# Kernel tuning notes

Hardware: AMD Instinct MI355X
Metric: run time of the kernel (lower is better)

The kernel has to match this reference:

```python
import jax, jax.numpy as jnp
import numpy as np

B, H, W, C = 4, 448, 448, 3
P = 16
G = 28            # grid = H // P
T = G * G         # 784 patches
E = 768
HD = 3072
NH = 12
DH = E // NH
L = 6
LW = 9            # local_window


def _ln(x, g, b, eps=1e-5):
    m = x.mean(-1, keepdims=True)
    v = ((x - m) ** 2).mean(-1, keepdims=True)
    return (x - m) / jnp.sqrt(v + eps) * g + b


def _mask_bias():
    # torch bool attn_mask: True = disallowed. The module sets True for LOCAL
    # neighbors (|dr|<=lw//2 and |dc|<=lw//2), so local positions are MASKED OUT.
    idx = jnp.arange(T)
    r, c = idx // G, idx % G
    local = (jnp.abs(r[:, None] - r[None, :]) <= LW // 2) & \
            (jnp.abs(c[:, None] - c[None, :]) <= LW // 2)
    return jnp.where(local, -jnp.inf, 0.0).astype(jnp.float32)  # [T, T]


def _img_to_patch(x):
    # x: [B,H,W,C] -> [B,T,C*P*P], channel-major within a patch (matches torch code)
    x = x.transpose(0, 3, 1, 2)                       # [B,C,H,W]
    x = x.reshape(B, C, G, P, G, P)
    x = x.transpose(0, 2, 4, 1, 3, 5)                 # [B,G,G,C,P,P]
    return x.reshape(B, T, C * P * P)


def _forward(x, sxr_mean, sxr_std, input_w, input_b, pos_emb,
             ln1_w, ln1_b, in_w, in_b, out_w, out_b, ln2_w, ln2_b,
             w1, b1, w2, b2, head_ln_w, head_ln_b, head_w, head_b):
    h = _img_to_patch(x) @ input_w.T + input_b        # [B,T,E]
    h = (h.reshape(B, G, G, E) + pos_emb).reshape(B, T, E)
    bias = _mask_bias()

    def block(h, prm):
        l1w, l1b, iw, ib, ow, ob, l2w, l2b, W1, B1, W2, B2 = prm
        y = _ln(h, l1w, l1b)
        qkv = y @ iw.T + ib                           # [B,T,3E]
        q, k, v = jnp.split(qkv, 3, axis=-1)
        q = q.reshape(B, T, NH, DH)
        k = k.reshape(B, T, NH, DH)
        v = v.reshape(B, T, NH, DH)
        s = jnp.einsum('bqhd,bkhd->bhqk', q, k) / jnp.sqrt(jnp.float32(DH)) + bias
        a = jax.nn.softmax(s, axis=-1)
        o = jnp.einsum('bhqk,bkhd->bqhd', a, v).reshape(B, T, E)
        h = h + o @ ow.T + ob
        y2 = _ln(h, l2w, l2b)
        m = jax.nn.gelu(y2 @ W1.T + B1, approximate=False)  # torch nn.GELU default
        h = h + m @ W2.T + B2
        return h, None

    h, _ = jax.lax.scan(block, h, (ln1_w, ln1_b, in_w, in_b, out_w, out_b,
                                   ln2_w, ln2_b, w1, b1, w2, b2))

    logits = (_ln(h, head_ln_w, head_ln_b) @ head_w.T + head_b)[..., 0]  # [B,T]
    patch_flux = jnp.clip(10.0 ** (logits * sxr_std[0] + sxr_mean[0]) - 1e-8,
                          1e-15, 1.0)
    global_flux = jnp.maximum(patch_flux.sum(axis=1, keepdims=True), 1e-15)
    return global_flux, patch_flux


def setup_inputs() -> dict:
    key = jax.random.key(0)
    ks = iter(jax.random.split(key, 16))
    def p(shape, s=0.02):
        return jax.random.normal(next(ks), shape, jnp.float32) * s
    return dict(
        x=jax.random.normal(next(ks), (B, H, W, C), jnp.float32),
        sxr_mean=jnp.array([-6.0], jnp.float32),
        sxr_std=jnp.array([1.0], jnp.float32),
        input_w=p((E, C * P * P)), input_b=jnp.zeros(E, jnp.float32),
        pos_emb=p((1, G, G, E), 1.0),
        ln1_w=jnp.ones((L, E), jnp.float32), ln1_b=jnp.zeros((L, E), jnp.float32),
        in_w=p((L, 3 * E, E)), in_b=jnp.zeros((L, 3 * E), jnp.float32),
        out_w=p((L, E, E)), out_b=jnp.zeros((L, E), jnp.float32),
        ln2_w=jnp.ones((L, E), jnp.float32), ln2_b=jnp.zeros((L, E), jnp.float32),
        w1=p((L, HD, E)), b1=jnp.zeros((L, HD), jnp.float32),
        w2=p((L, E, HD)), b2=jnp.zeros((L, E), jnp.float32),
        head_ln_w=jnp.ones(E, jnp.float32), head_ln_b=jnp.zeros(E, jnp.float32),
        head_w=p((1, E)), head_b=jnp.zeros(1, jnp.float32),
    )


def reference(x, sxr_mean, sxr_std, input_w, input_b, pos_emb,
              ln1_w, ln1_b, in_w, in_b, out_w, out_b, ln2_w, ln2_b,
              w1, b1, w2, b2, head_ln_w, head_ln_b, head_w, head_b):
    return _forward(x, sxr_mean, sxr_std, input_w, input_b, pos_emb,
                    ln1_w, ln1_b, in_w, in_b, out_w, out_b, ln2_w, ln2_b,
                    w1, b1, w2, b2, head_ln_w, head_ln_b, head_w, head_b)
```

## Files before the change

### kernel.cpp

```cpp
#include <hip/hip_runtime.h>
#include <math.h>

#define BB 4
#define TT 784
#define GG 28
#define EE 768
#define HDIM 3072
#define NHEAD 12
#define NLAYER 6
#define TTP 832
#define PSL (3136 * 768)

typedef short bfrag __attribute__((ext_vector_type(8)));
typedef float ffrag __attribute__((ext_vector_type(4)));

__device__ __forceinline__ unsigned short f2b(float f) {
    union { float f; unsigned u; } v; v.f = f;
    unsigned r = v.u + 0x7FFF + ((v.u >> 16) & 1);
    return (unsigned short)(r >> 16);
}

__device__ __forceinline__ float fexp2(float x) {
    float r; asm("v_exp_f32 %0, %1" : "=v"(r) : "v"(x)); return r;
}
__device__ __forceinline__ float frcp(float x) {
    float r; asm("v_rcp_f32 %0, %1" : "=v"(r) : "v"(x)); return r;
}

#define GLOAD_LDS16(g, l)                                                          \
    __builtin_amdgcn_global_load_lds(                                              \
        (const __attribute__((address_space(1))) void*)(g),                        \
        (__attribute__((address_space(3))) void*)(l), 16, 0, 0)

__device__ __forceinline__ void swz_bxyz(int& bx, int& by, int& bz) {
    int gx = gridDim.x, gy = gridDim.y, gz = gridDim.z;
    int nwg = gx * gy * gz;
    int orig = blockIdx.x + gx * (blockIdx.y + gy * blockIdx.z);
    int q = nwg >> 3, r = nwg & 7;
    int xc = orig & 7, li = orig >> 3;
    int wg = (xc < r ? xc * (q + 1) : r * (q + 1) + (xc - r) * q) + li;
    bx = wg % gx;
    int t = wg / gx;
    by = t % gy;
    bz = t / gy;
}

__device__ __forceinline__ float block_reduce_sum256(float v, volatile float* sb) {
    #pragma unroll
    for (int m = 1; m < 64; m <<= 1) v += __shfl_xor(v, m, 64);
    int wave = threadIdx.x >> 6;
    if ((threadIdx.x & 63) == 0) sb[wave] = v;
    __syncthreads();
    return sb[0] + sb[1] + sb[2] + sb[3];
}

__device__ __forceinline__ float block_reduce_sum192(float v, volatile float* sb) {
    #pragma unroll
    for (int m = 1; m < 64; m <<= 1) v += __shfl_xor(v, m, 64);
    int wave = threadIdx.x >> 6;
    if ((threadIdx.x & 63) == 0) sb[wave] = v;
    __syncthreads();
    return sb[0] + sb[1] + sb[2];
}

__global__ __launch_bounds__(256) void cast_kernel(const float* __restrict__ s,
                                                   unsigned short* __restrict__ d, int n4) {
    int i = blockIdx.x * 256 + threadIdx.x;
    if (i >= n4) return;
    float4 v = ((const float4*)s)[i];
    ushort4 o;
    o.x = f2b(v.x); o.y = f2b(v.y); o.z = f2b(v.z); o.w = f2b(v.w);
    ((ushort4*)d)[i] = o;
}

__global__ __launch_bounds__(256) void fused_cast_kernel(const float* __restrict__ iw,
                                                         const float* __restrict__ ow,
                                                         const float* __restrict__ W1,
                                                         const float* __restrict__ W2,
                                                         unsigned short* __restrict__ dq,
                                                         unsigned short* __restrict__ doo,
                                                         unsigned short* __restrict__ d1,
                                                         unsigned short* __restrict__ d2) {
    int i = blockIdx.x * 256 + threadIdx.x;
    const float* s; unsigned short* d; int k;
    if (i < 442368)            { s = iw;  d = dq;  k = i; }
    else if (i < 589824)       { s = ow;  d = doo; k = i - 442368; }
    else if (i < 1179648)      { s = W1;  d = d1;  k = i - 589824; }
    else if (i < 1769472)      { s = W2;  d = d2;  k = i - 1179648; }
    else return;
    float4 v = ((const float4*)s)[k];
    ushort4 o;
    o.x = f2b(v.x); o.y = f2b(v.y); o.z = f2b(v.z); o.w = f2b(v.w);
    ((ushort4*)d)[k] = o;
}

__global__ __launch_bounds__(256) void patchify_kernel(const float* __restrict__ x,
                                                       unsigned short* __restrict__ P) {
    int idx = blockIdx.x * blockDim.x + threadIdx.x;
    const int total = BB * TT * EE;
    if (idx >= total) return;
    int k = idx % EE;
    int t = (idx / EE) % TT;
    int b = idx / (EE * TT);
    int c = k >> 8;
    int rem = k & 255;
    int p1 = rem >> 4;
    int p2 = rem & 15;
    int g1 = t / GG, g2 = t % GG;
    int hh = g1 * 16 + p1, ww = g2 * 16 + p2;
    P[idx] = f2b(x[((b * 448 + hh) * 448 + ww) * 3 + c]);
}

__global__ __launch_bounds__(256) void posfill_kernel(float* __restrict__ h,
                                                      const float* __restrict__ pos) {
    int idx = blockIdx.x * blockDim.x + threadIdx.x;
    const int total = BB * TT * EE;
    if (idx >= total) return;
    h[idx] = pos[idx % (TT * EE)];
}

__global__ __launch_bounds__(256) void mask_build_kernel(unsigned long long* __restrict__ mt) {
    int idx = blockIdx.x * 256 + threadIdx.x;
    if (idx >= TT * 13) return;
    int row = idx / 13, t = idx % 13;
    int qr = row / GG, qc = row % GG;
    unsigned long long bits = 0;
    for (int i = 0; i < 64; i++) {
        int k = t * 64 + i;
        bool m;
        if (k >= TT) m = true;
        else {
            int kr2 = k / GG, kc2 = k % GG;
            m = (abs(qr - kr2) <= 4) && (abs(qc - kc2) <= 4);
        }
        if (m) bits |= (1ull << i);
    }
    mt[idx] = bits;
}

__global__ __launch_bounds__(192) void ln_red_kernel(float* __restrict__ H,
                                                     const float* __restrict__ P,
                                                     const float* __restrict__ g,
                                                     const float* __restrict__ bt,
                                                     unsigned short* __restrict__ Yb,
                                                     float* __restrict__ Yf) {
    __shared__ float sb1[3];
    __shared__ float sb2[3];
    int row = blockIdx.x, tid = threadIdx.x;
    size_t base = (size_t)row * EE + tid * 4;
    float4 hv = *(float4*)(H + base);
    float4 p0 = *(const float4*)(P + base);
    float4 p1 = *(const float4*)(P + (size_t)PSL + base);
    float4 p2 = *(const float4*)(P + 2 * (size_t)PSL + base);
    float4 p3 = *(const float4*)(P + 3 * (size_t)PSL + base);
    hv.x += (p0.x + p1.x) + (p2.x + p3.x);
    hv.y += (p0.y + p1.y) + (p2.y + p3.y);
    hv.z += (p0.z + p1.z) + (p2.z + p3.z);
    hv.w += (p0.w + p1.w) + (p2.w + p3.w);
    *(float4*)(H + base) = hv;
    float s = block_reduce_sum192((hv.x + hv.y) + (hv.z + hv.w), sb1);
    float mean = s * (1.0f / 768.0f);
    float dx = hv.x - mean, dy = hv.y - mean, dz = hv.z - mean, dw = hv.w - mean;
    __syncthreads();
    float ss = block_reduce_sum192((dx * dx + dy * dy) + (dz * dz + dw * dw), sb2);
    float rstd = rsqrtf(ss * (1.0f / 768.0f) + 1e-5f);
    float4 gv = *(const float4*)(g + tid * 4);
    float4 bv = *(const float4*)(bt + tid * 4);
    float y0 = dx * rstd * gv.x + bv.x;
    float y1 = dy * rstd * gv.y + bv.y;
    float y2 = dz * rstd * gv.z + bv.z;
    float y3 = dw * rstd * gv.w + bv.w;
    ushort4 o;
    o.x = f2b(y0); o.y = f2b(y1); o.z = f2b(y2); o.w = f2b(y3);
    *(ushort4*)(Yb + base) = o;
    if (Yf) {
        float4 yf; yf.x = y0; yf.y = y1; yf.z = y2; yf.w = y3;
        *(float4*)(Yf + base) = yf;
    }
}

__device__ __forceinline__ void gemm_core(const unsigned short* __restrict__ A,
                                          const unsigned short* __restrict__ W,
                                          int M, int K, int m0, int n0,
                                          int kbeg, int nk,
                                          unsigned short* As,
                                          unsigned short* Ws,
                                          ffrag (&acc)[4][4]) {
    int tid = threadIdx.x;
    int wave = tid >> 6, lane = tid & 63;
    int cl = lane & 15, qd = lane >> 4;
    int sr  = lane >> 2;
    int sbk = lane & 3;
    int ssc = (sbk ^ (sr & 3)) << 3;
    int mh = (wave & 1) << 6, nh = (wave >> 1) << 6;

    const unsigned short* Asrc0;
    const unsigned short* Asrc1;
    const unsigned short* Wsrc0;
    const unsigned short* Wsrc1;
    {
        int ar0 = m0 + (wave << 5) + sr;       if (ar0 > M - 1) ar0 = M - 1;
        int ar1 = m0 + (wave << 5) + 16 + sr;  if (ar1 > M - 1) ar1 = M - 1;
        Asrc0 = A + (size_t)ar0 * K + kbeg + ssc;
        Asrc1 = A + (size_t)ar1 * K + kbeg + ssc;
        int wr0 = n0 + (wave << 5) + sr;
        int wr1 = n0 + (wave << 5) + 16 + sr;
        Wsrc0 = W + (size_t)wr0 * K + kbeg + ssc;
        Wsrc1 = W + (size_t)wr1 * K + kbeg + ssc;
    }
    int dof0 = (wave << 10);
    int dof1 = (wave << 10) + 512;
    int fo = (qd ^ (cl & 3)) << 3;

#define STAGE32(sa, sw, kk) do {                         \
        GLOAD_LDS16(Asrc0 + (kk), (sa) + dof0);          \
        GLOAD_LDS16(Asrc1 + (kk), (sa) + dof1);          \
        GLOAD_LDS16(Wsrc0 + (kk), (sw) + dof0);          \
        GLOAD_LDS16(Wsrc1 + (kk), (sw) + dof1);          \
    } while (0)

    unsigned short *a0 = As, *a1 = As + 4096, *a2 = As + 8192;
    unsigned short *w0 = Ws, *w1 = Ws + 4096, *w2 = Ws + 8192;

    STAGE32(a0, w0, 0);
    if (nk > 1) STAGE32(a1, w1, 32);

    for (int t = 0; t < nk; ++t) {
        if (t + 2 < nk) {
            STAGE32(a2, w2, (t + 2) << 5);
            asm volatile("s_waitcnt vmcnt(8)" ::: "memory");
        } else if (t + 1 < nk) {
            asm volatile("s_waitcnt vmcnt(4)" ::: "memory");
        } else {
            asm volatile("s_waitcnt vmcnt(0)" ::: "memory");
        }
        __builtin_amdgcn_s_barrier();
        __builtin_amdgcn_sched_barrier(0);

        bfrag af[4], bf[4];
        #pragma unroll
        for (int i = 0; i < 4; i++)
            af[i] = *(const bfrag*)&a0[((mh + (i << 4) + cl) << 5) + fo];
        #pragma unroll
        for (int j = 0; j < 4; j++)
            bf[j] = *(const bfrag*)&w0[((nh + (j << 4) + cl) << 5) + fo];
        __builtin_amdgcn_s_setprio(1);
        #pragma unroll
        for (int i = 0; i < 4; i++)
            #pragma unroll
            for (int j = 0; j < 4; j++)
                acc[i][j] = __builtin_amdgcn_mfma_f32_16x16x32_bf16(af[i], bf[j], acc[i][j], 0, 0, 0);
        __builtin_amdgcn_s_setprio(0);

        __builtin_amdgcn_s_barrier();
        unsigned short* tp;
        tp = a0; a0 = a1; a1 = a2; a2 = tp;
        tp = w0; w0 = w1; w1 = w2; w2 = tp;
    }
#undef STAGE32
}

__global__ __launch_bounds__(256) void gemm_bf16(const unsigned short* __restrict__ A,
                                                 const unsigned short* __restrict__ W,
                                                 const float* __restrict__ bias,
                                                 const float* R, float* C,
                                                 unsigned short* Cb,
                                                 int M, int N, int K, int act) {
    __shared__ __align__(16) unsigned short As[3 * 4096];
    __shared__ __align__(16) unsigned short Ws[3 * 4096];
    int bx, by, bz;
    swz_bxyz(bx, by, bz);
    int m0 = by << 7, n0 = bx << 7;

    ffrag acc[4][4] = {};
    gemm_core(A, W, M, K, m0, n0, 0, K >> 5, As, Ws, acc);

    int tid = threadIdx.x;
    int wave = tid >> 6, lane = tid & 63;
    int cl = lane & 15, qd = lane >> 4;
    int mh = (wave & 1) << 6, nh = (wave >> 1) << 6;

    #pragma unroll
    for (int j = 0; j < 4; j++) {
        int col = n0 + nh + (j << 4) + cl;
        float bv = bias[col];
        #pragma unroll
        for (int i = 0; i < 4; i++) {
            int row0 = m0 + mh + (i << 4) + (qd << 2);
            #pragma unroll
            for (int r = 0; r < 4; r++) {
                int row = row0 + r;
                if (row < M) {
                    float v = acc[i][j][r] + bv;
                    if (R) v += R[(size_t)row * N + col];
                    if (act) v = 0.5f * v * (1.0f + erff(v * 0.70710678118654752f));
                    if (C)  C[(size_t)row * N + col] = v;
                    if (Cb) Cb[(size_t)row * N + col] = f2b(v);
                }
            }
        }
    }
}

__global__ __launch_bounds__(256) void gemm_qkv(const unsigned short* __restrict__ A,
                                                const unsigned short* __restrict__ W,
                                                const float* __restrict__ bias,
                                                unsigned short* __restrict__ Q,
                                                unsigned short* __restrict__ Kd,
                                                unsigned short* __restrict__ vT,
                                                int M, int N, int K) {
    __shared__ __align__(16) unsigned short As[3 * 4096];
    __shared__ __align__(16) unsigned short Ws[3 * 4096];
    int bx, by, bz;
    swz_bxyz(bx, by, bz);
    int m0 = by << 7, n0 = bx << 7;

    ffrag acc[4][4] = {};
    gemm_core(A, W, M, K, m0, n0, 0, K >> 5, As, Ws, acc);

    int tid = threadIdx.x;
    int wave = tid >> 6, lane = tid & 63;
    int cl = lane & 15, qd = lane >> 4;
    int mh = (wave & 1) << 6, nh = (wave >> 1) << 6;

    int ncb = n0 + nh;
    if (ncb < 1536) {
        unsigned short* dst = (ncb < 768) ? Q : Kd;
        int cb = (ncb < 768) ? 0 : 768;
        #pragma unroll
        for (int j = 0; j < 4; j++) {
            int col = ncb + (j << 4) + cl;
            float bv = bias[col];
            #pragma unroll
            for (int i = 0; i < 4; i++) {
                int row0 = m0 + mh + (i << 4) + (qd << 2);
                #pragma unroll
                for (int r = 0; r < 4; r++) {
                    int row = row0 + r;
                    if (row < M)
                        dst[(size_t)row * EE + col - cb] = f2b(acc[i][j][r] + bv);
                }
            }
        }
    } else {
        int hh = (ncb - 1536) >> 6;
        #pragma unroll
        for (int i = 0; i < 4; i++) {
            int row0 = m0 + mh + (i << 4) + (qd << 2);
            #pragma unroll
            for (int r = 0; r < 4; r++) {
                int row = row0 + r;
                if (row < M) {
                    int b = row / TT;
                    int t = row - b * TT;
                    size_t vbase = ((size_t)(b * NHEAD + hh) * 64) * TTP + t;
                    #pragma unroll
                    for (int j = 0; j < 4; j++) {
                        int col = ncb + (j << 4) + cl;
                        vT[vbase + (size_t)((j << 4) + cl) * TTP] =
                            f2b(acc[i][j][r] + bias[col]);
                    }
                }
            }
        }
    }
}

__global__ __launch_bounds__(256) void gemm_bf16_pk(const unsigned short* __restrict__ A,
                                                    const unsigned short* __restrict__ W,
                                                    const float* __restrict__ bias,
                                                    float* __restrict__ Pp,
                                                    int M, int N, int K, int KC) {
    __shared__ __align__(16) unsigned short As[3 * 4096];
    __shared__ __align__(16) unsigned short Ws[3 * 4096];
    int bx, by, bz;
    swz_bxyz(bx, by, bz);
    int m0 = by << 7, n0 = bx << 7;
    int z = bz;
    int kbeg = z * KC;
    int kc2 = (kbeg + KC > K) ? (K - kbeg) : KC;

    ffrag acc[4][4] = {};
    gemm_core(A, W, M, K, m0, n0, kbeg, kc2 >> 5, As, Ws, acc);

    int tid = threadIdx.x;
    int wave = tid >> 6, lane = tid & 63;
    int cl = lane & 15, qd = lane >> 4;
    int mh = (wave & 1) << 6, nh = (wave >> 1) << 6;
    float* Cz = Pp + (size_t)z * M * N;

    #pragma unroll
    for (int j = 0; j < 4; j++) {
        int col = n0 + nh + (j << 4) + cl;
        float bv = (z == 0) ? bias[col] : 0.0f;
        #pragma unroll
        for (int i = 0; i < 4; i++) {
            int row0 = m0 + mh + (i << 4) + (qd << 2);
            #pragma unroll
            for (int r = 0; r < 4; r++) {
                int row = row0 + r;
                if (row < M)
                    Cz[(size_t)row * N + col] = acc[i][j][r] + bv;
            }
        }
    }
}

#define LP 72
#define SCL2 0.18033688011112042f
__global__ __launch_bounds__(256) void attn_kernel(const unsigned short* __restrict__ Qg,
                                                   const unsigned short* __restrict__ Kg,
                                                   const unsigned short* __restrict__ vT,
                                                   const unsigned long long* __restrict__ mtab,
                                                   unsigned short* __restrict__ O) {
    __shared__ unsigned short Ks[64 * LP];
    __shared__ unsigned short Vt[80 * LP];
    __shared__ unsigned short Pb[64 * LP];
    int tid = threadIdx.x;
    int wave = tid >> 6, lane = tid & 63;
    int cl = lane & 15, qd = lane >> 4;
    int bx, by, bz;
    swz_bxyz(bx, by, bz);
    int bh = by;
    int b = bh / NHEAD, hh = bh % NHEAD;
    int q0 = bx * 64;
    int qw = q0 + wave * 16;

    for (int i = tid; i < 16 * LP; i += 256)
        Vt[64 * LP + i] = (i < LP) ? (unsigned short)0x3F80 : (unsigned short)0;

    int qrow = qw + cl;
    if (qrow > TT - 1) qrow = TT - 1;
    const unsigned short* qb = Qg + (size_t)(b * TT + qrow) * EE + hh * 64;
    bfrag qf0 = *(const bfrag*)(qb + (qd << 3));
    bfrag qf1 = *(const bfrag*)(qb + 32 + (qd << 3));

    ffrag o_acc[5] = {};
    float m_run[4];
    int qg_[4], qm_[4];
    #pragma unroll
    for (int r = 0; r < 4; r++) {
        qg_[r] = qw + (qd << 2) + r;
        qm_[r] = qg_[r] > TT - 1 ? TT - 1 : qg_[r];
        m_run[r] = -1e30f;
    }

    const unsigned short* kbase = Kg + (size_t)b * TT * EE + hh * 64;
    const unsigned short* vbase = vT + (size_t)(b * NHEAD + hh) * 64 * TTP;
    int srow = tid >> 3;
    int scol = (tid & 7) << 3;
    int r0 = srow, r1 = 32 + srow;
    const unsigned short* vp0 = vbase + (size_t)r0 * TTP + scol;
    const unsigned short* vp1 = vbase + (size_t)r1 * TTP + scol;

    bfrag kreg0 = *(const bfrag*)(kbase + (size_t)r0 * EE + scol);
    bfrag kreg1 = *(const bfrag*)(kbase + (size_t)r1 * EE + scol);
    bfrag vreg0 = *(const bfrag*)vp0;
    bfrag vreg1 = *(const bfrag*)vp1;

    int rot = (cl >> 2) & 3;
    int pread0 = (wave * 16 + cl) * LP + ((((qd >> 1)    ) ^ rot) << 4) + ((qd & 1) << 3);
    int pread1 = (wave * 16 + cl) * LP + (((2 + (qd >> 1)) ^ rot) << 4) + ((qd & 1) << 3);

    for (int k0 = 0; k0 < 832; k0 += 64) {
        __syncthreads();
        *(bfrag*)&Ks[r0 * LP + scol] = kreg0;
        *(bfrag*)&Ks[r1 * LP + scol] = kreg1;
        *(bfrag*)&Vt[r0 * LP + scol] = vreg0;
        *(bfrag*)&Vt[r1 * LP + scol] = vreg1;

        int tix = k0 >> 6;
        unsigned mlo[4], mhi[4];
        #pragma unroll
        for (int r = 0; r < 4; r++) {
            unsigned long long mb = mtab[qm_[r] * 13 + tix];
            mlo[r] = (unsigned)mb;
            mhi[r] = (unsigned)(mb >> 32);
        }
        __syncthreads();

        if (k0 + 64 < 832) {
            int kn = k0 + 64;
            int t0 = kn + r0; if (t0 > TT - 1) t0 = TT - 1;
            int t1 = kn + r1; if (t1 > TT - 1) t1 = TT - 1;
            kreg0 = *(const bfrag*)(kbase + (size_t)t0 * EE + scol);
            kreg1 = *(const bfrag*)(kbase + (size_t)t1 * EE + scol);
            vreg0 = *(const bfrag*)(vp0 + kn);
            vreg1 = *(const bfrag*)(vp1 + kn);
        }

        ffrag sv[4];
        #pragma unroll
        for (int j = 0; j < 4; j++) {
            bfrag kf0 = *(const bfrag*)&Ks[(j * 16 + cl) * LP + (qd << 3)];
            bfrag kf1 = *(const bfrag*)&Ks[(j * 16 + cl) * LP + 32 + (qd << 3)];
            ffrag z = {0.f, 0.f, 0.f, 0.f};
            z = __builtin_amdgcn_mfma_f32_16x16x32_bf16(qf0, kf0, z, 0, 0, 0);
            z = __builtin_amdgcn_mfma_f32_16x16x32_bf16(qf1, kf1, z, 0, 0, 0);
            sv[j] = z;
        }

        #pragma unroll
        for (int j = 0; j < 4; j++) {
            #pragma unroll
            for (int r = 0; r < 4; r++) {
                unsigned sel = (j < 2) ? mlo[r] : mhi[r];
                if ((sel >> (((j & 1) << 4) + cl)) & 1) sv[j][r] = -3.0e38f;
            }
        }

        #pragma unroll
        for (int r = 0; r < 4; r++) {
            float mx = fmaxf(fmaxf(sv[0][r], sv[1][r]), fmaxf(sv[2][r], sv[3][r]));
            mx = fmaxf(mx, __shfl_xor(mx, 1, 64));
            mx = fmaxf(mx, __shfl_xor(mx, 2, 64));
            mx = fmaxf(mx, __shfl_xor(mx, 4, 64));
            mx = fmaxf(mx, __shfl_xor(mx, 8, 64));
            float m_new = fmaxf(m_run[r], mx);
            float alpha = fexp2((m_run[r] - m_new) * SCL2);
            float p0 = fexp2((sv[0][r] - m_new) * SCL2);
            float p1 = fexp2((sv[1][r] - m_new) * SCL2);
            float p2 = fexp2((sv[2][r] - m_new) * SCL2);
            float p3 = fexp2((sv[3][r] - m_new) * SCL2);
            m_run[r] = m_new;
            #pragma unroll
            for (int t = 0; t < 5; t++) o_acc[t][r] *= alpha;
            int prow = (wave * 16 + (qd << 2) + r) * LP;
            Pb[prow + ((0 ^ qd) << 4) + cl] = f2b(p0);
            Pb[prow + ((1 ^ qd) << 4) + cl] = f2b(p1);
            Pb[prow + ((2 ^ qd) << 4) + cl] = f2b(p2);
            Pb[prow + ((3 ^ qd) << 4) + cl] = f2b(p3);
        }
        asm volatile("s_waitcnt lgkmcnt(0)" ::: "memory");

        bfrag pf0 = *(const bfrag*)&Pb[pread0];
        bfrag pf1 = *(const bfrag*)&Pb[pread1];
        #pragma unroll
        for (int t = 0; t < 5; t++) {
            bfrag vf0 = *(const bfrag*)&Vt[(t * 16 + cl) * LP + (qd << 3)];
            bfrag vf1 = *(const bfrag*)&Vt[(t * 16 + cl) * LP + 32 + (qd << 3)];
            o_acc[t] = __builtin_amdgcn_mfma_f32_16x16x32_bf16(pf0, vf0, o_acc[t], 0, 0, 0);
            o_acc[t] = __builtin_amdgcn_mfma_f32_16x16x32_bf16(pf1, vf1, o_acc[t], 0, 0, 0);
        }
    }

    #pragma unroll
    for (int r = 0; r < 4; r++) {
        float l = __shfl(o_acc[4][r], lane & 48, 64);
        float inv = frcp(fmaxf(l, 1e-30f));
        if (qg_[r] < TT) {
            #pragma unroll
            for (int t = 0; t < 4; t++)
                O[(size_t)(b * TT + qg_[r]) * EE + hh * 64 + t * 16 + cl] =
                    f2b(o_acc[t][r] * inv);
        }
    }
}

__global__ __launch_bounds__(256) void head_kernel(const float* __restrict__ Y,
                                                   const float* __restrict__ hw,
                                                   const float* __restrict__ hb,
                                                   const float* __restrict__ mean_,
                                                   const float* __restrict__ std_,
                                                   float* __restrict__ out) {
    __shared__ float sb[4];
    int row = blockIdx.x;
    int tid = threadIdx.x;
    const float* y = Y + (size_t)row * EE;
    float v = y[tid] * hw[tid] + y[tid + 256] * hw[tid + 256] + y[tid + 512] * hw[tid + 512];
    v = block_reduce_sum256(v, sb);
    if (tid == 0) {
        float logit = v + hb[0];
        float z = logit * std_[0] + mean_[0];
        float f = expf(z * 2.302585092994046f) - 1e-8f;
        f = fminf(fmaxf(f, 1e-15f), 1.0f);
        out[4 + row] = f;
    }
}

__global__ __launch_bounds__(256) void flux_sum_kernel(float* __restrict__ out) {
    __shared__ float sb[4];
    int b = blockIdx.x;
    int tid = threadIdx.x;
    const float* pf = out + 4 + (size_t)b * TT;
    float v = pf[tid] + pf[tid + 256] + pf[tid + 512];
    if (tid < TT - 768) v += pf[tid + 768];
    v = block_reduce_sum256(v, sb);
    if (tid == 0) out[b] = fmaxf(v, 1e-15f);
}

extern "C" void kernel_launch(void* const* d_in, const int* in_sizes, int n_in,
                              void* d_out, int out_size, void* d_ws, size_t ws_size,
                              hipStream_t stream) {
    const float* x        = (const float*)d_in[0];
    const float* sxr_mean = (const float*)d_in[1];
    const float* sxr_std  = (const float*)d_in[2];
    const float* input_w  = (const float*)d_in[3];
    const float* input_b  = (const float*)d_in[4];
    const float* pos_emb  = (const float*)d_in[5];
    const float* ln1_w    = (const float*)d_in[6];
    const float* ln1_b    = (const float*)d_in[7];
    const float* in_w     = (const float*)d_in[8];
    const float* in_b     = (const float*)d_in[9];
    const float* out_w    = (const float*)d_in[10];
    const float* out_b    = (const float*)d_in[11];
    const float* ln2_w    = (const float*)d_in[12];
    const float* ln2_b    = (const float*)d_in[13];
    const float* w1       = (const float*)d_in[14];
    const float* b1       = (const float*)d_in[15];
    const float* w2       = (const float*)d_in[16];
    const float* b2       = (const float*)d_in[17];
    const float* head_ln_w = (const float*)d_in[18];
    const float* head_ln_b = (const float*)d_in[19];
    const float* head_w   = (const float*)d_in[20];
    const float* head_b   = (const float*)d_in[21];
    float* out = (float*)d_out;

    const size_t NROW = (size_t)BB * TT;
    const size_t NE   = NROW * EE;

    float* h   = (float*)d_ws;
    float* y32 = h + NE;
    unsigned short* q_b   = (unsigned short*)(y32 + NE);
    unsigned short* k_b   = q_b + NE;
    unsigned short* vT_b  = k_b + NE;
    unsigned short* y_b   = vT_b + (size_t)BB * NHEAD * 64 * TTP;
    unsigned short* o_b   = y_b + NE;
    unsigned short* mlp_b = o_b + NE;
    unsigned short* wq_b  = mlp_b + NROW * HDIM;
    unsigned short* wo_b  = wq_b + (size_t)3 * EE * EE;
    unsigned short* w1_b  = wo_b + (size_t)EE * EE;
    unsigned short* w2_b  = w1_b + (size_t)HDIM * EE;
    unsigned long long* mtab = (unsigned long long*)(w2_b + (size_t)EE * HDIM);
    float* Pp = (float*)(mtab + TT * 13);

    const int tot = BB * TT * EE;
    const int GY = (int)((NROW + 127) / 128);

    patchify_kernel<<<(tot + 255) / 256, 256, 0, stream>>>(x, mlp_b);
    cast_kernel<<<(EE * EE / 4 + 255) / 256, 256, 0, stream>>>(input_w, wo_b, EE * EE / 4);
    posfill_kernel<<<(tot + 255) / 256, 256, 0, stream>>>(h, pos_emb);
    mask_build_kernel<<<(TT * 13 + 255) / 256, 256, 0, stream>>>(mtab);
    gemm_bf16_pk<<<dim3(EE / 128, GY, 4), 256, 0, stream>>>(
        mlp_b, wo_b, input_b, Pp, (int)NROW, EE, EE, 192);

    for (int l = 0; l < NLAYER; l++) {
        fused_cast_kernel<<<6912, 256, 0, stream>>>(
            in_w + (size_t)l * 3 * EE * EE, out_w + (size_t)l * EE * EE,
            w1 + (size_t)l * HDIM * EE, w2 + (size_t)l * EE * HDIM,
            wq_b, wo_b, w1_b, w2_b);

        ln_red_kernel<<<(int)NROW, 192, 0, stream>>>(
            h, Pp, ln1_w + l * EE, ln1_b + l * EE, y_b, nullptr);
        gemm_qkv<<<dim3(3 * EE / 128, GY), 256, 0, stream>>>(
            y_b, wq_b, in_b + (size_t)l * 3 * EE, q_b, k_b, vT_b,
            (int)NROW, 3 * EE, EE);
        attn_kernel<<<dim3(13, BB * NHEAD), 256, 0, stream>>>(q_b, k_b, vT_b, mtab, o_b);
        gemm_bf16_pk<<<dim3(EE / 128, GY, 4), 256, 0, stream>>>(
            o_b, wo_b, out_b + (size_t)l * EE, Pp, (int)NROW, EE, EE, 192);
        ln_red_kernel<<<(int)NROW, 192, 0, stream>>>(
            h, Pp, ln2_w + l * EE, ln2_b + l * EE, y_b, nullptr);
        gemm_bf16<<<dim3(HDIM / 128, GY), 256, 0, stream>>>(
            y_b, w1_b, b1 + (size_t)l * HDIM, nullptr, nullptr, mlp_b,
            (int)NROW, HDIM, EE, 1);
        gemm_bf16_pk<<<dim3(EE / 128, GY, 4), 256, 0, stream>>>(
            mlp_b, w2_b, b2 + (size_t)l * EE, Pp, (int)NROW, EE, HDIM, 768);
    }

    ln_red_kernel<<<(int)NROW, 192, 0, stream>>>(
        h, Pp, head_ln_w, head_ln_b, y_b, y32);
    head_kernel<<<(int)NROW, 256, 0, stream>>>(y32, head_w, head_b, sxr_mean, sxr_std, out);
    flux_sum_kernel<<<BB, 256, 0, stream>>>(out);
}
```

Baseline: 1.418 ms.

## Split GEMM tiles across eight waves with a fragment-major LDS layout

The shared bf16 GEMM core now runs with 512 threads per block. Each of eight waves computes a 64x32 sub-tile instead of four waves computing 64x64. Staging is one 16-row chunk per wave per operand, stored in a fragment-major LDS layout read contiguously, which replaces the XOR-swizzled layout. The aim is more waves in flight to hide load latency and fewer accumulator registers per thread. In exchange, each wave issues half as many MFMAs between barriers, so synchronisation overhead rises relative to compute.

Measured after the change: 1.528 ms. 7.8% more time.

```diff
diff --git a/kernel.cpp b/kernel.cpp
--- a/kernel.cpp
+++ b/kernel.cpp
@@ -185,38 +185,30 @@
                                           int kbeg, int nk,
                                           unsigned short* As,
                                           unsigned short* Ws,
-                                          ffrag (&acc)[4][4]) {
+                                          ffrag (&acc)[4][2]) {
     int tid = threadIdx.x;
     int wave = tid >> 6, lane = tid & 63;
     int cl = lane & 15, qd = lane >> 4;
-    int sr  = lane >> 2;
-    int sbk = lane & 3;
-    int ssc = (sbk ^ (sr & 3)) << 3;
-    int mh = (wave & 1) << 6, nh = (wave >> 1) << 6;
-
-    const unsigned short* Asrc0;
-    const unsigned short* Asrc1;
-    const unsigned short* Wsrc0;
-    const unsigned short* Wsrc1;
+    int srow = lane & 15;
+    int sblk = lane >> 4;
+    int gm = (wave & 1) << 2;
+    int gn = (wave >> 1);
+
+    int gn2 = (wave >> 1) << 1;
+
+    const unsigned short* Asrc;
+    const unsigned short* Wsrc;
     {
-        int ar0 = m0 + (wave << 5) + sr;       if (ar0 > M - 1) ar0 = M - 1;
-        int ar1 = m0 + (wave << 5) + 16 + sr;  if (ar1 > M - 1) ar1 = M - 1;
-        Asrc0 = A + (size_t)ar0 * K + kbeg + ssc;
-        Asrc1 = A + (size_t)ar1 * K + kbeg + ssc;
-        int wr0 = n0 + (wave << 5) + sr;
-        int wr1 = n0 + (wave << 5) + 16 + sr;
-        Wsrc0 = W + (size_t)wr0 * K + kbeg + ssc;
-        Wsrc1 = W + (size_t)wr1 * K + kbeg + ssc;
-    }
-    int dof0 = (wave << 10);
-    int dof1 = (wave << 10) + 512;
-    int fo = (qd ^ (cl & 3)) << 3;
+        int ar = m0 + (wave << 4) + srow;  if (ar > M - 1) ar = M - 1;
+        Asrc = A + (size_t)ar * K + kbeg + (sblk << 3);
+        int wr = n0 + (wave << 4) + srow;
+        Wsrc = W + (size_t)wr * K + kbeg + (sblk << 3);
+    }
+    int dof = wave << 9;
 
 #define STAGE32(sa, sw, kk) do {                         \
-        GLOAD_LDS16(Asrc0 + (kk), (sa) + dof0);          \
-        GLOAD_LDS16(Asrc1 + (kk), (sa) + dof1);          \
-        GLOAD_LDS16(Wsrc0 + (kk), (sw) + dof0);          \
-        GLOAD_LDS16(Wsrc1 + (kk), (sw) + dof1);          \
+        GLOAD_LDS16(Asrc + (kk), (sa) + dof);            \
+        GLOAD_LDS16(Wsrc + (kk), (sw) + dof);            \
     } while (0)
 
     unsigned short *a0 = As, *a1 = As + 4096, *a2 = As + 8192;
@@ -224,31 +216,33 @@
 
     STAGE32(a0, w0, 0);
     if (nk > 1) STAGE32(a1, w1, 32);
+
+    int roff = (qd << 7) + (cl << 3);
 
     for (int t = 0; t < nk; ++t) {
         if (t + 2 < nk) {
             STAGE32(a2, w2, (t + 2) << 5);
-            asm volatile("s_waitcnt vmcnt(8)" ::: "memory");
+            asm volatile("s_waitcnt vmcnt(4)" ::: "memory");
         } else if (t + 1 < nk) {
-            asm volatile("s_waitcnt vmcnt(4)" ::: "memory");
+            asm volatile("s_waitcnt vmcnt(2)" ::: "memory");
         } else {
             asm volatile("s_waitcnt vmcnt(0)" ::: "memory");
         }
         __builtin_amdgcn_s_barrier();
         __builtin_amdgcn_sched_barrier(0);
 
-        bfrag af[4], bf[4];
+        bfrag af[4], bf[2];
         #pragma unroll
         for (int i = 0; i < 4; i++)
-            af[i] = *(const bfrag*)&a0[((mh + (i << 4) + cl) << 5) + fo];
-        #pragma unroll
-        for (int j = 0; j < 4; j++)
-            bf[j] = *(const bfrag*)&w0[((nh + (j << 4) + cl) << 5) + fo];
+            af[i] = *(const bfrag*)&a0[((gm + i) << 9) + roff];
+        #pragma unroll
+        for (int j = 0; j < 2; j++)
+            bf[j] = *(const bfrag*)&w0[((gn2 + j) << 9) + roff];
         __builtin_amdgcn_s_setprio(1);
         #pragma unroll
         for (int i = 0; i < 4; i++)
             #pragma unroll
-            for (int j = 0; j < 4; j++)
+            for (int j = 0; j < 2; j++)
                 acc[i][j] = __builtin_amdgcn_mfma_f32_16x16x32_bf16(af[i], bf[j], acc[i][j], 0, 0, 0);
         __builtin_amdgcn_s_setprio(0);
 
@@ -258,9 +252,10 @@
         tp = w0; w0 = w1; w1 = w2; w2 = tp;
     }
 #undef STAGE32
-}
-
-__global__ __launch_bounds__(256) void gemm_bf16(const unsigned short* __restrict__ A,
+    (void)gn;
+}
+
+__global__ __launch_bounds__(512) void gemm_bf16(const unsigned short* __restrict__ A,
                                                  const unsigned short* __restrict__ W,
                                                  const float* __restrict__ bias,
                                                  const float* R, float* C,
@@ -272,16 +267,16 @@
     swz_bxyz(bx, by, bz);
     int m0 = by << 7, n0 = bx << 7;
 
-    ffrag acc[4][4] = {};
+    ffrag acc[4][2] = {};
     gemm_core(A, W, M, K, m0, n0, 0, K >> 5, As, Ws, acc);
 
     int tid = threadIdx.x;
     int wave = tid >> 6, lane = tid & 63;
     int cl = lane & 15, qd = lane >> 4;
-    int mh = (wave & 1) << 6, nh = (wave >> 1) << 6;
+    int mh = (wave & 1) << 6, nh = (wave >> 1) << 5;
 
     #pragma unroll
-    for (int j = 0; j < 4; j++) {
+    for (int j = 0; j < 2; j++) {
         int col = n0 + nh + (j << 4) + cl;
         float bv = bias[col];
         #pragma unroll
@@ -302,7 +297,7 @@
     }
 }
 
-__global__ __launch_bounds__(256) void gemm_qkv(const unsigned short* __restrict__ A,
+__global__ __launch_bounds__(512) void gemm_qkv(const unsigned short* __restrict__ A,
                                                 const unsigned short* __restrict__ W,
                                                 const float* __restrict__ bias,
                                                 unsigned short* __restrict__ Q,
@@ -315,20 +310,20 @@
     swz_bxyz(bx, by, bz);
     int m0 = by << 7, n0 = bx << 7;
 
-    ffrag acc[4][4] = {};
+    ffrag acc[4][2] = {};
     gemm_core(A, W, M, K, m0, n0, 0, K >> 5, As, Ws, acc);
 
     int tid = threadIdx.x;
     int wave = tid >> 6, lane = tid & 63;
     int cl = lane & 15, qd = lane >> 4;
-    int mh = (wave & 1) << 6, nh = (wave >> 1) << 6;
+    int mh = (wave & 1) << 6, nh = (wave >> 1) << 5;
 
     int ncb = n0 + nh;
     if (ncb < 1536) {
         unsigned short* dst = (ncb < 768) ? Q : Kd;
         int cb = (ncb < 768) ? 0 : 768;
         #pragma unroll
-        for (int j = 0; j < 4; j++) {
+        for (int j = 0; j < 2; j++) {
             int col = ncb + (j << 4) + cl;
             float bv = bias[col];
             #pragma unroll
@@ -355,9 +350,9 @@
                     int t = row - b * TT;
                     size_t vbase = ((size_t)(b * NHEAD + hh) * 64) * TTP + t;
                     #pragma unroll
-                    for (int j = 0; j < 4; j++) {
+                    for (int j = 0; j < 2; j++) {
                         int col = ncb + (j << 4) + cl;
-                        vT[vbase + (size_t)((j << 4) + cl) * TTP] =
+                        vT[vbase + (size_t)(col - 1536 - hh * 64) * TTP] =
                             f2b(acc[i][j][r] + bias[col]);
                     }
                 }
@@ -366,7 +361,7 @@
     }
 }
 
-__global__ __launch_bounds__(256) void gemm_bf16_pk(const unsigned short* __restrict__ A,
+__global__ __launch_bounds__(512) void gemm_bf16_pk(const unsigned short* __restrict__ A,
                                                     const unsigned short* __restrict__ W,
                                                     const float* __restrict__ bias,
                                                     float* __restrict__ Pp,
@@ -380,17 +375,17 @@
     int kbeg = z * KC;
     int kc2 = (kbeg + KC > K) ? (K - kbeg) : KC;
 
-    ffrag acc[4][4] = {};
+    ffrag acc[4][2] = {};
     gemm_core(A, W, M, K, m0, n0, kbeg, kc2 >> 5, As, Ws, acc);
 
     int tid = threadIdx.x;
     int wave = tid >> 6, lane = tid & 63;
     int cl = lane & 15, qd = lane >> 4;
-    int mh = (wave & 1) << 6, nh = (wave >> 1) << 6;
+    int mh = (wave & 1) << 6, nh = (wave >> 1) << 5;
     float* Cz = Pp + (size_t)z * M * N;
 
     #pragma unroll
-    for (int j = 0; j < 4; j++) {
+    for (int j = 0; j < 2; j++) {
         int col = n0 + nh + (j << 4) + cl;
         float bv = (z == 0) ? bias[col] : 0.0f;
         #pragma unroll
@@ -641,7 +636,7 @@
     cast_kernel<<<(EE * EE / 4 + 255) / 256, 256, 0, stream>>>(input_w, wo_b, EE * EE / 4);
     posfill_kernel<<<(tot + 255) / 256, 256, 0, stream>>>(h, pos_emb);
     mask_build_kernel<<<(TT * 13 + 255) / 256, 256, 0, stream>>>(mtab);
-    gemm_bf16_pk<<<dim3(EE / 128, GY, 4), 256, 0, stream>>>(
+    gemm_bf16_pk<<<dim3(EE / 128, GY, 4), 512, 0, stream>>>(
         mlp_b, wo_b, input_b, Pp, (int)NROW, EE, EE, 192);
 
     for (int l = 0; l < NLAYER; l++) {
@@ -652,18 +647,18 @@
 
         ln_red_kernel<<<(int)NROW, 192, 0, stream>>>(
             h, Pp, ln1_w + l * EE, ln1_b + l * EE, y_b, nullptr);
-        gemm_qkv<<<dim3(3 * EE / 128, GY), 256, 0, stream>>>(
+        gemm_qkv<<<dim3(3 * EE / 128, GY), 512, 0, stream>>>(
             y_b, wq_b, in_b + (size_t)l * 3 * EE, q_b, k_b, vT_b,
             (int)NROW, 3 * EE, EE);
         attn_kernel<<<dim3(13, BB * NHEAD), 256, 0, stream>>>(q_b, k_b, vT_b, mtab, o_b);
-        gemm_bf16_pk<<<dim3(EE / 128, GY, 4), 256, 0, stream>>>(
+        gemm_bf16_pk<<<dim3(EE / 128, GY, 4), 512, 0, stream>>>(
             o_b, wo_b, out_b + (size_t)l * EE, Pp, (int)NROW, EE, EE, 192);
         ln_red_kernel<<<(int)NROW, 192, 0, stream>>>(
             h, Pp, ln2_w + l * EE, ln2_b + l * EE, y_b, nullptr);
-        gemm_bf16<<<dim3(HDIM / 128, GY), 256, 0, stream>>>(
+        gemm_bf16<<<dim3(HDIM / 128, GY), 512, 0, stream>>>(
             y_b, w1_b, b1 + (size_t)l * HDIM, nullptr, nullptr, mlp_b,
             (int)NROW, HDIM, EE, 1);
-        gemm_bf16_pk<<<dim3(EE / 128, GY, 4), 256, 0, stream>>>(
+        gemm_bf16_pk<<<dim3(EE / 128, GY, 4), 512, 0, stream>>>(
             mlp_b, w2_b, b2 + (size_t)l * EE, Pp, (int)NROW, EE, HDIM, 768);
     }
 
```
